# Optimization experiments

Hardware: AMD Instinct MI355X
Metric: run time of the kernel (lower is better)

The kernel has to match this reference:

```python
import jax, jax.numpy as jnp
import numpy as np

L = 10
DIM = 4
TABLE = 1 << 16
BASE_RES = 16.0
PLS = 2.0
HID = 64
SCALE_MULTI = 0.5
DENSITY_OFFSET = -1.0
SCENE_SCALING = 2.0
PRIMES = (np.uint32(1), np.uint32(2654435761), np.uint32(805459861))


def _safe_exp(x):
    return jnp.exp(jnp.clip(x, -30.0, 10.0))


def _l2norm(x, eps=1e-8):
    return x / jnp.sqrt(jnp.sum(x * x, -1, keepdims=True) + eps)


def _circumcenters(tets):
    # tets: [T,4,3]; solve 2(vi-v0).c = |vi|^2-|v0|^2
    v0 = tets[:, 0]
    A = 2.0 * (tets[:, 1:] - v0[:, None, :]) + 1e-6 * jnp.eye(3, dtype=tets.dtype)
    b = jnp.sum(tets[:, 1:] ** 2, -1) - jnp.sum(v0 ** 2, -1)[:, None]
    c = jnp.linalg.solve(A, b[..., None])[..., 0]
    r = jnp.linalg.norm(c - v0, axis=-1)
    return c, r


def _project_to_tet(p, tets):
    # clamp-and-renormalize barycentric coordinates (approximate projection)
    v0 = tets[:, 0]
    E = tets[:, 1:] - v0[:, None, :]
    M = jnp.einsum('tid,tjd->tij', E, E) + 1e-6 * jnp.eye(3, dtype=tets.dtype)
    rhs = jnp.einsum('tid,td->ti', E, p - v0)
    lam = jnp.linalg.solve(M, rhs[..., None])[..., 0]
    bary = jnp.concatenate([1.0 - lam.sum(-1, keepdims=True), lam], -1)
    bary = jnp.clip(bary, 0.0, 1.0)
    bary = bary / jnp.clip(bary.sum(-1, keepdims=True), 1e-6, None)
    return jnp.einsum('tv,tvd->td', bary, tets)


def _contract_mean_std(x, std):
    # mipnerf-360 style scene contraction of mean; std scaled by |J| ~ 1/n^2
    n = jnp.maximum(jnp.linalg.norm(x, axis=-1, keepdims=True), 1e-9)
    cx = jnp.where(n <= 1.0, x, (2.0 - 1.0 / n) * x / n)
    cs = std * jnp.where(n[..., 0] <= 1.0, 1.0, 1.0 / (n[..., 0] ** 2))
    return cx, cs


def _hash_encode(pos, tables):
    # pos [T,3] in [0,1); tables [L, TABLE, DIM]; multiresolution hash grid
    mask = np.uint32(TABLE - 1)
    pos = jnp.clip(pos, 0.0, 1.0 - 1e-6)
    feats = []
    for l in range(L):
        res = float(np.floor(BASE_RES * (PLS ** l)))
        x = pos * res
        f = jnp.floor(x)
        w = x - f
        fi = f.astype(jnp.uint32)
        acc = jnp.zeros(pos.shape[:-1] + (DIM,), pos.dtype)
        for cz in (0, 1):
            for cy in (0, 1):
                for cx in (0, 1):
                    c = fi + jnp.asarray((cx, cy, cz), jnp.uint32)
                    h = ((c[..., 0] * PRIMES[0]) ^ (c[..., 1] * PRIMES[1]) ^ (c[..., 2] * PRIMES[2])) & mask
                    wt = ((w[..., 0] if cx else 1.0 - w[..., 0]) *
                          (w[..., 1] if cy else 1.0 - w[..., 1]) *
                          (w[..., 2] if cz else 1.0 - w[..., 2]))
                    acc = acc + tables[l][h.astype(jnp.int32)] * wt[..., None]
        feats.append(acc)
    return jnp.stack(feats, axis=1)  # [T, L, DIM]


def _forward(vertices, indices, center, tables, W1, b1, W2, b2, W3, b3):
    tets = vertices[indices]  # [T,4,3] gather
    cc, radius = _circumcenters(tets)
    cc = _project_to_tet(cc, tets)
    normalized = (cc - center) / SCENE_SCALING
    cv, cr = _contract_mean_std(normalized, radius / SCENE_SCALING)
    cr = cr * SCALE_MULTI
    n = jnp.arange(L, dtype=vertices.dtype)
    erf_x = 1.0 / jnp.sqrt(PLS * 4.0 * n[None, :] * cr[:, None] + 1e-12)
    scaling = jax.lax.erf(erf_x)  # [T, L] per-level erf anti-aliasing scale
    pos = cv * 0.25 + 0.5  # contracted [-2,2] -> [0,1]
    feats = _hash_encode(pos, tables) * scaling[..., None]
    h = feats.reshape(feats.shape[0], L * DIM)
    h = jax.nn.selu(h @ W1 + b1)
    h = jax.nn.selu(h @ W2 + b2)
    out = h @ W3 + b3  # [T, 13]
    density = _safe_exp(out[:, 0] + DENSITY_OFFSET)
    pairs = ((0, 1), (0, 2), (0, 3), (1, 2), (1, 3), (2, 3))
    el = jnp.stack([jnp.linalg.norm(tets[:, i] - tets[:, j], axis=1) for i, j in pairs], 0).max(0)
    alpha = 1.0 - jnp.exp(-density * el)
    V = vertices.shape[0]
    vertex_alpha = jnp.zeros((V,), vertices.dtype).at[indices].max(
        jnp.broadcast_to(alpha[:, None], indices.shape))  # scatter amax
    fs = out[:, 1:]
    base = fs[:, :3] + 0.5
    grads = jnp.clip(base[:, :, None], 0.0, None) * jnp.tanh(fs[:, 3:12].reshape(-1, 3, 3))
    offs = _l2norm(tets - cc[:, None, :])
    vcol = base[:, None, :] + jnp.einsum('tcd,tvd->tvc', grads, offs)  # [T,4,3]
    return vertex_alpha, vcol


def setup_inputs() -> dict:
    key = jax.random.key(0)
    ks = jax.random.split(key, 8)
    V, T = 100000, 500000
    vertices = jax.random.normal(ks[0], (V, 3), jnp.float32) * 0.5
    indices = jax.random.randint(ks[1], (T, 4), 0, V, jnp.int32)
    center = jnp.zeros((1, 3), jnp.float32)
    tables = jax.random.normal(ks[2], (L, TABLE, DIM), jnp.float32) * 1e-2
    def lin(k, i, o):
        s = (6.0 / (i + o)) ** 0.5
        return jax.random.uniform(k, (i, o), jnp.float32, -s, s)
    return dict(vertices=vertices, indices=indices, center=center, tables=tables,
                W1=lin(ks[3], L * DIM, HID), b1=jnp.zeros((HID,), jnp.float32),
                W2=lin(ks[4], HID, HID), b2=jnp.zeros((HID,), jnp.float32),
                W3=lin(ks[5], HID, 13), b3=jnp.zeros((13,), jnp.float32))


def reference(vertices, indices, center, tables, W1, b1, W2, b2, W3, b3):
    return _forward(vertices, indices, center, tables, W1, b1, W2, b2, W3, b3)
```

## Files before the change

kernel.cpp:

```cpp
#include <hip/hip_runtime.h>
#include <math.h>

#define NLVL 10
#define TBL 65536
#define NHID 64
#define NIN 40
#define LDP 68

typedef __attribute__((ext_vector_type(8))) short bf16x8;
typedef __attribute__((ext_vector_type(4))) float f32x4;
typedef unsigned int uint;
typedef unsigned short ushort;

__device__ __forceinline__ float selu_f(float x) {
    return 1.0507009873554805f * (x > 0.0f ? x : 1.6732632423543772f * (__expf(x) - 1.0f));
}
__device__ __forceinline__ float fast_tanh(float x) {
    float xx = fminf(fmaxf(x, -15.0f), 15.0f);
    float t = __expf(2.0f * xx);
    return (t - 1.0f) / (t + 1.0f);
}
__device__ __forceinline__ short2 tsplit(float x) {
    uint u = __float_as_uint(x);
    short hi = (short)(u >> 16);
    float hif = __uint_as_float(u & 0xFFFF0000u);
    float lo = x - hif;
    short los = (short)(__float_as_uint(lo) >> 16);
    short2 s; s.x = hi; s.y = los;
    return s;
}

__device__ __forceinline__ void solve3d(const double A[3][3], const double b[3], double x[3]) {
    double a00=A[0][0], a01=A[0][1], a02=A[0][2];
    double a10=A[1][0], a11=A[1][1], a12=A[1][2];
    double a20=A[2][0], a21=A[2][1], a22=A[2][2];
    double C00 =  (a11*a22 - a12*a21);
    double C01 = -(a10*a22 - a12*a20);
    double C02 =  (a10*a21 - a11*a20);
    double C10 = -(a01*a22 - a02*a21);
    double C11 =  (a00*a22 - a02*a20);
    double C12 = -(a00*a21 - a01*a20);
    double C20 =  (a01*a12 - a02*a11);
    double C21 = -(a00*a12 - a02*a10);
    double C22 =  (a00*a11 - a01*a10);
    double det = a00*C00 + a01*C01 + a02*C02;
    double inv = 1.0 / det;
    x[0] = (C00*b[0] + C10*b[1] + C20*b[2]) * inv;
    x[1] = (C01*b[0] + C11*b[1] + C21*b[2]) * inv;
    x[2] = (C02*b[0] + C12*b[1] + C22*b[2]) * inv;
}

__global__ void __launch_bounds__(256) zero_alpha_kernel(float* out, int V) {
    int i = blockIdx.x * blockDim.x + threadIdx.x;
    if (i < V) out[i] = 0.0f;
}

__device__ __forceinline__ void enc2(const float4* __restrict__ tb4,
                                     float px, float py, float pz, float crf,
                                     int l0, float f[8]) {
    uint idx[2][8];
    float wt[2][8];
    #pragma unroll
    for (int h = 0; h < 2; ++h) {
        int l = l0 + h;
        float res = (float)(16 << l);
        float x0 = px*res, x1 = py*res, x2 = pz*res;
        float f0 = floorf(x0), f1 = floorf(x1), f2 = floorf(x2);
        float w0 = x0-f0, w1 = x1-f1, w2 = x2-f2;
        uint i0 = (uint)f0, i1 = (uint)f1, i2 = (uint)f2;
        #pragma unroll
        for (int cn = 0; cn < 8; ++cn) {
            uint cx = (uint)(cn & 1), cy = (uint)((cn >> 1) & 1), cz = (uint)((cn >> 2) & 1);
            idx[h][cn] = (((i0 + cx) * 1u) ^ ((i1 + cy) * 2654435761u) ^ ((i2 + cz) * 805459861u)) & 65535u;
            wt[h][cn] = (cx ? w0 : 1.0f - w0) * (cy ? w1 : 1.0f - w1) * (cz ? w2 : 1.0f - w2);
        }
    }
    float4 v[2][8];
    #pragma unroll
    for (int h = 0; h < 2; ++h)
        #pragma unroll
        for (int cn = 0; cn < 8; ++cn)
            v[h][cn] = tb4[(size_t)(l0+h)*TBL + idx[h][cn]];
    #pragma unroll
    for (int h = 0; h < 2; ++h) {
        float a0=0.f, a1=0.f, a2=0.f, a3=0.f;
        #pragma unroll
        for (int cn = 0; cn < 8; ++cn) {
            float w = wt[h][cn];
            a0 = fmaf(v[h][cn].x, w, a0);
            a1 = fmaf(v[h][cn].y, w, a1);
            a2 = fmaf(v[h][cn].z, w, a2);
            a3 = fmaf(v[h][cn].w, w, a3);
        }
        float sc = erff(rsqrtf(8.0f*(float)(l0+h)*crf + 1e-12f));
        f[h*4+0] = a0*sc; f[h*4+1] = a1*sc; f[h*4+2] = a2*sc; f[h*4+3] = a3*sc;
    }
}

__device__ __forceinline__ void store_split8(const float f[8],
                                             ushort* __restrict__ fh,
                                             ushort* __restrict__ fl) {
    bf16x8 h8, l8;
    #pragma unroll
    for (int j = 0; j < 8; ++j) {
        short2 sp = tsplit(f[j]);
        h8[j] = sp.x; l8[j] = sp.y;
    }
    *reinterpret_cast<bf16x8*>(fh) = h8;
    *reinterpret_cast<bf16x8*>(fl) = l8;
}

__global__ void __launch_bounds__(256) geom01_kernel(
    const float* __restrict__ vertices,
    const int*   __restrict__ indices,
    const float* __restrict__ center,
    const float* __restrict__ tables,
    float* __restrict__ aux,
    ushort* __restrict__ feats_hi,
    ushort* __restrict__ feats_lo, int T)
{
    int t = blockIdx.x * blockDim.x + threadIdx.x;
    if (t >= T) return;

    double p[4][3];
    #pragma unroll
    for (int v = 0; v < 4; ++v) {
        int vid = indices[t*4+v];
        p[v][0] = (double)vertices[vid*3+0];
        p[v][1] = (double)vertices[vid*3+1];
        p[v][2] = (double)vertices[vid*3+2];
    }

    double A[3][3], bb[3];
    double v0sq = p[0][0]*p[0][0] + p[0][1]*p[0][1] + p[0][2]*p[0][2];
    #pragma unroll
    for (int i = 0; i < 3; ++i) {
        #pragma unroll
        for (int j = 0; j < 3; ++j)
            A[i][j] = 2.0*(p[i+1][j] - p[0][j]) + (i==j ? 1e-6 : 0.0);
        bb[i] = p[i+1][0]*p[i+1][0] + p[i+1][1]*p[i+1][1] + p[i+1][2]*p[i+1][2] - v0sq;
    }
    double c[3];
    solve3d(A, bb, c);
    double dx0 = c[0]-p[0][0], dy0 = c[1]-p[0][1], dz0 = c[2]-p[0][2];
    double radius = sqrt(dx0*dx0 + dy0*dy0 + dz0*dz0);

    double E[3][3];
    #pragma unroll
    for (int i = 0; i < 3; ++i)
        #pragma unroll
        for (int j = 0; j < 3; ++j)
            E[i][j] = p[i+1][j] - p[0][j];
    double M[3][3], rhs[3];
    #pragma unroll
    for (int i = 0; i < 3; ++i) {
        #pragma unroll
        for (int k = 0; k < 3; ++k)
            M[i][k] = E[i][0]*E[k][0] + E[i][1]*E[k][1] + E[i][2]*E[k][2] + (i==k ? 1e-6 : 0.0);
        rhs[i] = E[i][0]*dx0 + E[i][1]*dy0 + E[i][2]*dz0;
    }
    double lam[3];
    solve3d(M, rhs, lam);
    double bary[4];
    bary[0] = 1.0 - lam[0] - lam[1] - lam[2];
    bary[1] = lam[0]; bary[2] = lam[1]; bary[3] = lam[2];
    double bs = 0.0;
    #pragma unroll
    for (int v = 0; v < 4; ++v) {
        bary[v] = fmin(fmax(bary[v], 0.0), 1.0);
        bs += bary[v];
    }
    bs = fmax(bs, 1e-6);
    double cc[3];
    #pragma unroll
    for (int j = 0; j < 3; ++j)
        cc[j] = (bary[0]*p[0][j] + bary[1]*p[1][j] + bary[2]*p[2][j] + bary[3]*p[3][j]) / bs;

    double xv[3];
    xv[0] = (cc[0] - (double)center[0]) * 0.5;
    xv[1] = (cc[1] - (double)center[1]) * 0.5;
    xv[2] = (cc[2] - (double)center[2]) * 0.5;
    double nrm = sqrt(xv[0]*xv[0] + xv[1]*xv[1] + xv[2]*xv[2]);
    double n = fmax(nrm, 1e-9);
    double cv[3], cs;
    if (n <= 1.0) {
        cv[0]=xv[0]; cv[1]=xv[1]; cv[2]=xv[2];
        cs = radius * 0.5;
    } else {
        double f = (2.0 - 1.0/n) / n;
        cv[0]=xv[0]*f; cv[1]=xv[1]*f; cv[2]=xv[2]*f;
        cs = radius * 0.5 / (n*n);
    }
    float crf = (float)(cs * 0.5);

    float px = fminf(fmaxf((float)(cv[0]*0.25 + 0.5), 0.0f), 1.0f - 1e-6f);
    float py = fminf(fmaxf((float)(cv[1]*0.25 + 0.5), 0.0f), 1.0f - 1e-6f);
    float pz = fminf(fmaxf((float)(cv[2]*0.25 + 0.5), 0.0f), 1.0f - 1e-6f);

    float el = 0.0f;
    #pragma unroll
    for (int a = 0; a < 3; ++a)
        #pragma unroll
        for (int bq = a+1; bq < 4; ++bq) {
            float ddx = (float)(p[a][0]-p[bq][0]);
            float ddy = (float)(p[a][1]-p[bq][1]);
            float ddz = (float)(p[a][2]-p[bq][2]);
            el = fmaxf(el, sqrtf(ddx*ddx + ddy*ddy + ddz*ddz));
        }

    size_t st = (size_t)T;
    aux[0*st + t] = px;
    aux[1*st + t] = py;
    aux[2*st + t] = pz;
    aux[3*st + t] = crf;
    aux[4*st + t] = (float)cc[0];
    aux[5*st + t] = (float)cc[1];
    aux[6*st + t] = (float)cc[2];
    aux[7*st + t] = el;

    const float4* tb4 = reinterpret_cast<const float4*>(tables);
    float f01[8];
    enc2(tb4, px, py, pz, crf, 0, f01);
    store_split8(f01, feats_hi + (size_t)t*NIN, feats_lo + (size_t)t*NIN);
}

template<int L0>
__global__ void __launch_bounds__(256) hash_pass_kernel(
    const float* __restrict__ tables,
    const float* __restrict__ aux,
    ushort* __restrict__ feats_hi,
    ushort* __restrict__ feats_lo, int T)
{
    int t = blockIdx.x * blockDim.x + threadIdx.x;
    if (t >= T) return;
    size_t st = (size_t)T;
    float px = aux[0*st + t];
    float py = aux[1*st + t];
    float pz = aux[2*st + t];
    float crf = aux[3*st + t];
    const float4* tb4 = reinterpret_cast<const float4*>(tables);

    float f[8];
    enc2(tb4, px, py, pz, crf, L0, f);
    store_split8(f, feats_hi + (size_t)t*NIN + L0*4, feats_lo + (size_t)t*NIN + L0*4);
}

__global__ void __launch_bounds__(256, 2) mlp_mfma_kernel(
    const ushort* __restrict__ feats_hi,
    const ushort* __restrict__ feats_lo,
    const float* __restrict__ aux,
    const float* __restrict__ vertices,
    const int*   __restrict__ indices,
    const float* __restrict__ W1, const float* __restrict__ b1,
    const float* __restrict__ W2, const float* __restrict__ b2,
    const float* __restrict__ W3, const float* __restrict__ b3,
    float* __restrict__ out, int T, int V)
{
    __shared__ __align__(16) float hts[4][16][LDP];

    const int tid  = threadIdx.x;
    const int wid  = tid >> 6;
    const int lane = tid & 63;
    const int r    = lane & 15;
    const int g    = lane >> 4;

    bf16x8 w1h[2][4];
    bf16x8 w1l0[4];
    #pragma unroll
    for (int s = 0; s < 2; ++s)
        #pragma unroll
        for (int nt = 0; nt < 4; ++nt) {
            bf16x8 h, lo;
            #pragma unroll
            for (int j = 0; j < 8; ++j) {
                int k = s*32 + g*8 + j;
                float w = (k < NIN) ? W1[k*NHID + nt*16 + r] : 0.0f;
                short2 sp = tsplit(w);
                h[j] = sp.x; lo[j] = sp.y;
            }
            w1h[s][nt] = h;
            if (s == 0) w1l0[nt] = lo;
        }
    bf16x8 w2h[2][4], w2l[2][4];
    #pragma unroll
    for (int s = 0; s < 2; ++s)
        #pragma unroll
        for (int nt = 0; nt < 4; ++nt) {
            bf16x8 h, lo;
            #pragma unroll
            for (int j = 0; j < 8; ++j) {
                int k = s*32 + g*8 + j;
                float w = W2[k*NHID + nt*16 + r];
                short2 sp = tsplit(w);
                h[j] = sp.x; lo[j] = sp.y;
            }
            w2h[s][nt] = h; w2l[s][nt] = lo;
        }
    bf16x8 w3h[2], w3l[2];
    #pragma unroll
    for (int s = 0; s < 2; ++s) {
        bf16x8 h, lo;
        #pragma unroll
        for (int j = 0; j < 8; ++j) {
            int k = s*32 + g*8 + j;
            float w = (r < 13) ? W3[k*13 + r] : 0.0f;
            short2 sp = tsplit(w);
            h[j] = sp.x; lo[j] = sp.y;
        }
        w3h[s] = h; w3l[s] = lo;
    }
    float b1v[4], b2v[4];
    #pragma unroll
    for (int nt = 0; nt < 4; ++nt) { b1v[nt] = b1[nt*16 + r]; b2v[nt] = b2[nt*16 + r]; }
    float b3v = (r < 13) ? b3[r] : 0.0f;

    const size_t st = (size_t)T;
    const int nmt = (T + 15) >> 4;
    const int gw = blockIdx.x * 4 + wid;
    const int gstride = gridDim.x * 4;

    for (int mt = gw; mt < nmt; mt += gstride) {
        const int t0 = mt * 16;
        const int trow = t0 + r;
        const bool rowok = trow < T;

        bf16x8 ah0, al0, ah1;
        {
            const bf16x8 z = {0,0,0,0,0,0,0,0};
            const ushort* fh = feats_hi + (size_t)trow * NIN;
            const ushort* fl = feats_lo + (size_t)trow * NIN;
            ah0 = rowok ? *reinterpret_cast<const bf16x8*>(fh + g*8) : z;
            al0 = rowok ? *reinterpret_cast<const bf16x8*>(fl + g*8) : z;
            ah1 = (rowok && g == 0) ? *reinterpret_cast<const bf16x8*>(fh + 32) : z;
        }

        #pragma unroll
        for (int nt = 0; nt < 4; ++nt) {
            f32x4 acc = {0.f, 0.f, 0.f, 0.f};
            acc = __builtin_amdgcn_mfma_f32_16x16x32_bf16(ah0, w1h[0][nt], acc, 0, 0, 0);
            acc = __builtin_amdgcn_mfma_f32_16x16x32_bf16(ah0, w1l0[nt],  acc, 0, 0, 0);
            acc = __builtin_amdgcn_mfma_f32_16x16x32_bf16(al0, w1h[0][nt], acc, 0, 0, 0);
            acc = __builtin_amdgcn_mfma_f32_16x16x32_bf16(ah1, w1h[1][nt], acc, 0, 0, 0);
            #pragma unroll
            for (int q = 0; q < 4; ++q)
                hts[wid][g*4 + q][nt*16 + r] = selu_f(acc[q] + b1v[nt]);
        }
        asm volatile("s_waitcnt lgkmcnt(0)" ::: "memory");

        bf16x8 a2h[2], a2l[2];
        #pragma unroll
        for (int s = 0; s < 2; ++s) {
            float4 u0 = *reinterpret_cast<const float4*>(&hts[wid][r][s*32 + g*8]);
            float4 u1 = *reinterpret_cast<const float4*>(&hts[wid][r][s*32 + g*8 + 4]);
            bf16x8 h, lo;
            short2 sp;
            sp = tsplit(u0.x); h[0]=sp.x; lo[0]=sp.y;
            sp = tsplit(u0.y); h[1]=sp.x; lo[1]=sp.y;
            sp = tsplit(u0.z); h[2]=sp.x; lo[2]=sp.y;
            sp = tsplit(u0.w); h[3]=sp.x; lo[3]=sp.y;
            sp = tsplit(u1.x); h[4]=sp.x; lo[4]=sp.y;
            sp = tsplit(u1.y); h[5]=sp.x; lo[5]=sp.y;
            sp = tsplit(u1.z); h[6]=sp.x; lo[6]=sp.y;
            sp = tsplit(u1.w); h[7]=sp.x; lo[7]=sp.y;
            a2h[s] = h; a2l[s] = lo;
        }
        asm volatile("s_waitcnt lgkmcnt(0)" ::: "memory");
        float h2v[4][4];
        #pragma unroll
        for (int nt = 0; nt < 4; ++nt) {
            f32x4 acc = {0.f, 0.f, 0.f, 0.f};
            #pragma unroll
            for (int s = 0; s < 2; ++s) {
                acc = __builtin_amdgcn_mfma_f32_16x16x32_bf16(a2h[s], w2h[s][nt], acc, 0, 0, 0);
                acc = __builtin_amdgcn_mfma_f32_16x16x32_bf16(a2h[s], w2l[s][nt], acc, 0, 0, 0);
                acc = __builtin_amdgcn_mfma_f32_16x16x32_bf16(a2l[s], w2h[s][nt], acc, 0, 0, 0);
            }
            #pragma unroll
            for (int q = 0; q < 4; ++q) h2v[nt][q] = selu_f(acc[q] + b2v[nt]);
        }
        #pragma unroll
        for (int nt = 0; nt < 4; ++nt)
            #pragma unroll
            for (int q = 0; q < 4; ++q)
                hts[wid][g*4 + q][nt*16 + r] = h2v[nt][q];
        asm volatile("s_waitcnt lgkmcnt(0)" ::: "memory");

        bf16x8 a3h[2], a3l[2];
        #pragma unroll
        for (int s = 0; s < 2; ++s) {
            float4 u0 = *reinterpret_cast<const float4*>(&hts[wid][r][s*32 + g*8]);
            float4 u1 = *reinterpret_cast<const float4*>(&hts[wid][r][s*32 + g*8 + 4]);
            bf16x8 h, lo;
            short2 sp;
            sp = tsplit(u0.x); h[0]=sp.x; lo[0]=sp.y;
            sp = tsplit(u0.y); h[1]=sp.x; lo[1]=sp.y;
            sp = tsplit(u0.z); h[2]=sp.x; lo[2]=sp.y;
            sp = tsplit(u0.w); h[3]=sp.x; lo[3]=sp.y;
            sp = tsplit(u1.x); h[4]=sp.x; lo[4]=sp.y;
            sp = tsplit(u1.y); h[5]=sp.x; lo[5]=sp.y;
            sp = tsplit(u1.z); h[6]=sp.x; lo[6]=sp.y;
            sp = tsplit(u1.w); h[7]=sp.x; lo[7]=sp.y;
            a3h[s] = h; a3l[s] = lo;
        }
        asm volatile("s_waitcnt lgkmcnt(0)" ::: "memory");
        {
            f32x4 acc = {0.f, 0.f, 0.f, 0.f};
            #pragma unroll
            for (int s = 0; s < 2; ++s) {
                acc = __builtin_amdgcn_mfma_f32_16x16x32_bf16(a3h[s], w3h[s], acc, 0, 0, 0);
                acc = __builtin_amdgcn_mfma_f32_16x16x32_bf16(a3h[s], w3l[s], acc, 0, 0, 0);
                acc = __builtin_amdgcn_mfma_f32_16x16x32_bf16(a3l[s], w3h[s], acc, 0, 0, 0);
            }
            #pragma unroll
            for (int q = 0; q < 4; ++q)
                hts[wid][g*4 + q][r] = acc[q] + b3v;
        }
        asm volatile("s_waitcnt lgkmcnt(0)" ::: "memory");

        {
            int et = lane >> 2;
            int ev = lane & 3;
            int te = t0 + et;
            if (te < T) {
                const float* orow = hts[wid][et];
                float4 o0 = *reinterpret_cast<const float4*>(&orow[0]);
                float4 o1 = *reinterpret_cast<const float4*>(&orow[4]);
                float4 o2 = *reinterpret_cast<const float4*>(&orow[8]);
                float o12 = orow[12];

                float el  = aux[7*st + te];
                float cc0 = aux[4*st + te], cc1 = aux[5*st + te], cc2 = aux[6*st + te];

                float dv = fminf(fmaxf(o0.x - 1.0f, -30.0f), 10.0f);
                float density = __expf(dv);
                float alpha = 1.0f - __expf(-density * el);
                int ab = __float_as_int(alpha);
                int vid = indices[te*4 + ev];
                atomicMax((int*)out + vid, ab);

                float base0 = o0.y + 0.5f, base1 = o0.z + 0.5f, base2 = o0.w + 0.5f;
                float bc0 = fmaxf(base0, 0.0f), bc1 = fmaxf(base1, 0.0f), bc2 = fmaxf(base2, 0.0f);
                float g00 = bc0*fast_tanh(o1.x), g01 = bc0*fast_tanh(o1.y), g02 = bc0*fast_tanh(o1.z);
                float g10 = bc1*fast_tanh(o1.w), g11 = bc1*fast_tanh(o2.x), g12 = bc1*fast_tanh(o2.y);
                float g20 = bc2*fast_tanh(o2.z), g21 = bc2*fast_tanh(o2.w), g22 = bc2*fast_tanh(o12);

                float pxv = vertices[vid*3+0], pyv = vertices[vid*3+1], pzv = vertices[vid*3+2];
                float ox = pxv-cc0, oy = pyv-cc1, oz = pzv-cc2;
                float inv = rsqrtf(ox*ox + oy*oy + oz*oz + 1e-8f);
                float q0 = ox*inv, q1 = oy*inv, q2 = oz*inv;
                float* vout = out + V + (size_t)te * 12 + ev*3;
                vout[0] = base0 + g00*q0 + g01*q1 + g02*q2;
                vout[1] = base1 + g10*q0 + g11*q1 + g12*q2;
                vout[2] = base2 + g20*q0 + g21*q1 + g22*q2;
            }
        }
        asm volatile("s_waitcnt lgkmcnt(0)" ::: "memory");
    }
}

__global__ void __launch_bounds__(256) tet_forward_fused(
    const float* __restrict__ vertices,
    const int*   __restrict__ indices,
    const float* __restrict__ center,
    const float* __restrict__ tables,
    const float* __restrict__ W1, const float* __restrict__ b1,
    const float* __restrict__ W2, const float* __restrict__ b2,
    const float* __restrict__ W3, const float* __restrict__ b3,
    float* __restrict__ out, int T, int V)
{
    int t = blockIdx.x * blockDim.x + threadIdx.x;
    if (t >= T) return;

    double p[4][3];
    int vv[4];
    #pragma unroll
    for (int v = 0; v < 4; ++v) {
        vv[v] = indices[t*4+v];
        p[v][0] = (double)vertices[vv[v]*3+0];
        p[v][1] = (double)vertices[vv[v]*3+1];
        p[v][2] = (double)vertices[vv[v]*3+2];
    }
    double A[3][3], bb[3];
    double v0sq = p[0][0]*p[0][0] + p[0][1]*p[0][1] + p[0][2]*p[0][2];
    #pragma unroll
    for (int i = 0; i < 3; ++i) {
        #pragma unroll
        for (int j = 0; j < 3; ++j)
            A[i][j] = 2.0*(p[i+1][j] - p[0][j]) + (i==j ? 1e-6 : 0.0);
        bb[i] = p[i+1][0]*p[i+1][0] + p[i+1][1]*p[i+1][1] + p[i+1][2]*p[i+1][2] - v0sq;
    }
    double c[3];
    solve3d(A, bb, c);
    double dx0 = c[0]-p[0][0], dy0 = c[1]-p[0][1], dz0 = c[2]-p[0][2];
    double radius = sqrt(dx0*dx0 + dy0*dy0 + dz0*dz0);
    double E[3][3];
    #pragma unroll
    for (int i = 0; i < 3; ++i)
        #pragma unroll
        for (int j = 0; j < 3; ++j)
            E[i][j] = p[i+1][j] - p[0][j];
    double M[3][3], rhs[3];
    #pragma unroll
    for (int i = 0; i < 3; ++i) {
        #pragma unroll
        for (int k = 0; k < 3; ++k)
            M[i][k] = E[i][0]*E[k][0] + E[i][1]*E[k][1] + E[i][2]*E[k][2] + (i==k ? 1e-6 : 0.0);
        rhs[i] = E[i][0]*dx0 + E[i][1]*dy0 + E[i][2]*dz0;
    }
    double lam[3];
    solve3d(M, rhs, lam);
    double bary[4];
    bary[0] = 1.0 - lam[0] - lam[1] - lam[2];
    bary[1] = lam[0]; bary[2] = lam[1]; bary[3] = lam[2];
    double bs = 0.0;
    #pragma unroll
    for (int v = 0; v < 4; ++v) { bary[v] = fmin(fmax(bary[v], 0.0), 1.0); bs += bary[v]; }
    bs = fmax(bs, 1e-6);
    double cc[3];
    #pragma unroll
    for (int j = 0; j < 3; ++j)
        cc[j] = (bary[0]*p[0][j] + bary[1]*p[1][j] + bary[2]*p[2][j] + bary[3]*p[3][j]) / bs;
    double xv[3];
    xv[0] = (cc[0] - (double)center[0]) * 0.5;
    xv[1] = (cc[1] - (double)center[1]) * 0.5;
    xv[2] = (cc[2] - (double)center[2]) * 0.5;
    double nrm = sqrt(xv[0]*xv[0] + xv[1]*xv[1] + xv[2]*xv[2]);
    double n = fmax(nrm, 1e-9);
    double cv[3], cs;
    if (n <= 1.0) { cv[0]=xv[0]; cv[1]=xv[1]; cv[2]=xv[2]; cs = radius * 0.5; }
    else { double f = (2.0 - 1.0/n) / n; cv[0]=xv[0]*f; cv[1]=xv[1]*f; cv[2]=xv[2]*f; cs = radius * 0.5 / (n*n); }
    float crf = (float)(cs * 0.5);
    float pos0 = fminf(fmaxf((float)(cv[0]*0.25 + 0.5), 0.0f), 1.0f - 1e-6f);
    float pos1 = fminf(fmaxf((float)(cv[1]*0.25 + 0.5), 0.0f), 1.0f - 1e-6f);
    float pos2 = fminf(fmaxf((float)(cv[2]*0.25 + 0.5), 0.0f), 1.0f - 1e-6f);

    float h0[NIN];
    float res = 16.0f;
    #pragma unroll
    for (int l = 0; l < NLVL; ++l) {
        float x0 = pos0*res, x1 = pos1*res, x2 = pos2*res;
        float f0 = floorf(x0), f1 = floorf(x1), f2 = floorf(x2);
        float w0 = x0-f0, w1 = x1-f1, w2 = x2-f2;
        unsigned i0 = (unsigned)f0, i1 = (unsigned)f1, i2 = (unsigned)f2;
        float a0=0.f, a1=0.f, a2=0.f, a3=0.f;
        #pragma unroll
        for (int cn = 0; cn < 8; ++cn) {
            unsigned cx = (unsigned)(cn & 1), cy = (unsigned)((cn >> 1) & 1), cz = (unsigned)((cn >> 2) & 1);
            unsigned hh = ((i0 + cx) * 1u) ^ ((i1 + cy) * 2654435761u) ^ ((i2 + cz) * 805459861u);
            hh &= 65535u;
            float wt = (cx ? w0 : 1.0f - w0) * (cy ? w1 : 1.0f - w1) * (cz ? w2 : 1.0f - w2);
            const float4 tv = *reinterpret_cast<const float4*>(tables + ((size_t)l*TBL + hh)*4);
            a0 = fmaf(tv.x, wt, a0); a1 = fmaf(tv.y, wt, a1);
            a2 = fmaf(tv.z, wt, a2); a3 = fmaf(tv.w, wt, a3);
        }
        float sc = erff(rsqrtf(8.0f*(float)l*crf + 1e-12f));
        h0[l*4+0] = a0*sc; h0[l*4+1] = a1*sc; h0[l*4+2] = a2*sc; h0[l*4+3] = a3*sc;
        res *= 2.0f;
    }

    float h1[NHID];
    #pragma unroll
    for (int j = 0; j < NHID; ++j) h1[j] = b1[j];
    #pragma unroll
    for (int i = 0; i < NIN; ++i) {
        float hi = h0[i];
        #pragma unroll
        for (int j = 0; j < NHID; ++j) h1[j] = fmaf(hi, W1[i*NHID + j], h1[j]);
    }
    #pragma unroll
    for (int j = 0; j < NHID; ++j) h1[j] = selu_f(h1[j]);

    float o[13];
    #pragma unroll
    for (int k = 0; k < 13; ++k) o[k] = b3[k];
    #pragma unroll
    for (int half = 0; half < 2; ++half) {
        float h2h[32];
        #pragma unroll
        for (int jj = 0; jj < 32; ++jj) h2h[jj] = b2[half*32 + jj];
        #pragma unroll
        for (int i = 0; i < NHID; ++i) {
            float hi = h1[i];
            #pragma unroll
            for (int jj = 0; jj < 32; ++jj)
                h2h[jj] = fmaf(hi, W2[i*NHID + half*32 + jj], h2h[jj]);
        }
        #pragma unroll
        for (int jj = 0; jj < 32; ++jj) {
            float hv = selu_f(h2h[jj]);
            #pragma unroll
            for (int k = 0; k < 13; ++k)
                o[k] = fmaf(hv, W3[(half*32 + jj)*13 + k], o[k]);
        }
    }

    float dv = fminf(fmaxf(o[0] - 1.0f, -30.0f), 10.0f);
    float density = __expf(dv);
    float el = 0.0f;
    #pragma unroll
    for (int a = 0; a < 3; ++a)
        #pragma unroll
        for (int bq = a+1; bq < 4; ++bq) {
            float ddx = (float)(p[a][0]-p[bq][0]);
            float ddy = (float)(p[a][1]-p[bq][1]);
            float ddz = (float)(p[a][2]-p[bq][2]);
            el = fmaxf(el, sqrtf(ddx*ddx + ddy*ddy + ddz*ddz));
        }
    float alpha = 1.0f - __expf(-density * el);
    int ab = __float_as_int(alpha);
    atomicMax((int*)out + vv[0], ab);
    atomicMax((int*)out + vv[1], ab);
    atomicMax((int*)out + vv[2], ab);
    atomicMax((int*)out + vv[3], ab);

    float base0 = o[1] + 0.5f, base1 = o[2] + 0.5f, base2 = o[3] + 0.5f;
    float bc0 = fmaxf(base0, 0.0f), bc1 = fmaxf(base1, 0.0f), bc2 = fmaxf(base2, 0.0f);
    float g00 = bc0*fast_tanh(o[4]),  g01 = bc0*fast_tanh(o[5]),  g02 = bc0*fast_tanh(o[6]);
    float g10 = bc1*fast_tanh(o[7]),  g11 = bc1*fast_tanh(o[8]),  g12 = bc1*fast_tanh(o[9]);
    float g20 = bc2*fast_tanh(o[10]), g21 = bc2*fast_tanh(o[11]), g22 = bc2*fast_tanh(o[12]);

    float* vout = out + V + (size_t)t * 12;
    #pragma unroll
    for (int v = 0; v < 4; ++v) {
        float ox = (float)(p[v][0]-cc[0]), oy = (float)(p[v][1]-cc[1]), oz = (float)(p[v][2]-cc[2]);
        float inv = rsqrtf(ox*ox + oy*oy + oz*oz + 1e-8f);
        float q0 = ox*inv, q1 = oy*inv, q2 = oz*inv;
        vout[v*3+0] = base0 + g00*q0 + g01*q1 + g02*q2;
        vout[v*3+1] = base1 + g10*q0 + g11*q1 + g12*q2;
        vout[v*3+2] = base2 + g20*q0 + g21*q1 + g22*q2;
    }
}

extern "C" void kernel_launch(void* const* d_in, const int* in_sizes, int n_in,
                              void* d_out, int out_size, void* d_ws, size_t ws_size,
                              hipStream_t stream) {
    const float* vertices = (const float*)d_in[0];
    const int*   indices  = (const int*)d_in[1];
    const float* center   = (const float*)d_in[2];
    const float* tables   = (const float*)d_in[3];
    const float* W1 = (const float*)d_in[4];
    const float* b1 = (const float*)d_in[5];
    const float* W2 = (const float*)d_in[6];
    const float* b2 = (const float*)d_in[7];
    const float* W3 = (const float*)d_in[8];
    const float* b3 = (const float*)d_in[9];
    int V = in_sizes[0] / 3;
    int T = in_sizes[1] / 4;
    float* out = (float*)d_out;

    hipLaunchKernelGGL(zero_alpha_kernel, dim3((V + 255) / 256), dim3(256), 0, stream, out, V);

    size_t need = (size_t)T * 48 * sizeof(float);
    dim3 grid((T + 255) / 256), blk(256);
    if (ws_size >= need) {
        float* aux = (float*)d_ws;
        ushort* feats_hi = (ushort*)(aux + (size_t)T * 8);
        ushort* feats_lo = feats_hi + (size_t)T * NIN;
        hipLaunchKernelGGL(geom01_kernel, grid, blk, 0, stream,
                           vertices, indices, center, tables, aux, feats_hi, feats_lo, T);
        hipLaunchKernelGGL((hash_pass_kernel<2>), grid, blk, 0, stream, tables, aux, feats_hi, feats_lo, T);
        hipLaunchKernelGGL((hash_pass_kernel<4>), grid, blk, 0, stream, tables, aux, feats_hi, feats_lo, T);
        hipLaunchKernelGGL((hash_pass_kernel<6>), grid, blk, 0, stream, tables, aux, feats_hi, feats_lo, T);
        hipLaunchKernelGGL((hash_pass_kernel<8>), grid, blk, 0, stream, tables, aux, feats_hi, feats_lo, T);
        hipLaunchKernelGGL(mlp_mfma_kernel, dim3(1024), blk, 0, stream, feats_hi, feats_lo, aux,
                           vertices, indices, W1, b1, W2, b2, W3, b3, out, T, V);
    } else {
        hipLaunchKernelGGL(tet_forward_fused, grid, blk, 0, stream,
                           vertices, indices, center, tables, W1, b1, W2, b2, W3, b3, out, T, V);
    }
}
```

Measured before the change: 236.8 us.

## Prefetch next tile features and epilogue gathers during MLP MFMA work

Software-pipelines the persistent MLP loop. Input feature fragments for the next tile are loaded while the current tile is being computed, and the per-tet indices, aux values and vertex gathers are issued early so their latency overlaps the MFMA layers. MFMA sections are also wrapped in s_setprio raises so their waves get issue priority. In exchange, more registers are live across the loop, which may lower occupancy.

```diff
diff --git a/kernel.cpp b/kernel.cpp
--- a/kernel.cpp
+++ b/kernel.cpp
@@ -318,22 +318,34 @@
     const int nmt = (T + 15) >> 4;
     const int gw = blockIdx.x * 4 + wid;
     const int gstride = gridDim.x * 4;
+    const bf16x8 zfrag = {0,0,0,0,0,0,0,0};
+
+    if (gw >= nmt) return;
+
+    bf16x8 ah0, al0, ah1;
+    {
+        int trow = gw*16 + r;
+        bool rowok = trow < T;
+        const ushort* fh = feats_hi + (size_t)trow * NIN;
+        const ushort* fl = feats_lo + (size_t)trow * NIN;
+        ah0 = rowok ? *reinterpret_cast<const bf16x8*>(fh + g*8) : zfrag;
+        al0 = rowok ? *reinterpret_cast<const bf16x8*>(fl + g*8) : zfrag;
+        ah1 = (rowok && g == 0) ? *reinterpret_cast<const bf16x8*>(fh + 32) : zfrag;
+    }
 
     for (int mt = gw; mt < nmt; mt += gstride) {
         const int t0 = mt * 16;
-        const int trow = t0 + r;
-        const bool rowok = trow < T;
-
-        bf16x8 ah0, al0, ah1;
-        {
-            const bf16x8 z = {0,0,0,0,0,0,0,0};
-            const ushort* fh = feats_hi + (size_t)trow * NIN;
-            const ushort* fl = feats_lo + (size_t)trow * NIN;
-            ah0 = rowok ? *reinterpret_cast<const bf16x8*>(fh + g*8) : z;
-            al0 = rowok ? *reinterpret_cast<const bf16x8*>(fl + g*8) : z;
-            ah1 = (rowok && g == 0) ? *reinterpret_cast<const bf16x8*>(fh + 32) : z;
-        }
-
+
+        const int te = t0 + (lane >> 2);
+        const int ev = lane & 3;
+        const bool teok = te < T;
+        int vid = teok ? indices[te*4 + ev] : 0;
+        float el  = teok ? aux[7*st + te] : 0.0f;
+        float cc0 = teok ? aux[4*st + te] : 0.0f;
+        float cc1 = teok ? aux[5*st + te] : 0.0f;
+        float cc2 = teok ? aux[6*st + te] : 0.0f;
+
+        __builtin_amdgcn_s_setprio(1);
         #pragma unroll
         for (int nt = 0; nt < 4; ++nt) {
             f32x4 acc = {0.f, 0.f, 0.f, 0.f};
@@ -345,6 +357,26 @@
             for (int q = 0; q < 4; ++q)
                 hts[wid][g*4 + q][nt*16 + r] = selu_f(acc[q] + b1v[nt]);
         }
+        __builtin_amdgcn_s_setprio(0);
+
+        const int mtn = mt + gstride;
+        bf16x8 nah0 = zfrag, nal0 = zfrag, nah1 = zfrag;
+        if (mtn < nmt) {
+            int trow = mtn*16 + r;
+            bool rowok = trow < T;
+            const ushort* fh = feats_hi + (size_t)trow * NIN;
+            const ushort* fl = feats_lo + (size_t)trow * NIN;
+            if (rowok) {
+                nah0 = *reinterpret_cast<const bf16x8*>(fh + g*8);
+                nal0 = *reinterpret_cast<const bf16x8*>(fl + g*8);
+                if (g == 0) nah1 = *reinterpret_cast<const bf16x8*>(fh + 32);
+            }
+        }
+
+        float pvx = vertices[vid*3+0];
+        float pvy = vertices[vid*3+1];
+        float pvz = vertices[vid*3+2];
+
         asm volatile("s_waitcnt lgkmcnt(0)" ::: "memory");
 
         bf16x8 a2h[2], a2l[2];
@@ -366,6 +398,7 @@
         }
         asm volatile("s_waitcnt lgkmcnt(0)" ::: "memory");
         float h2v[4][4];
+        __builtin_amdgcn_s_setprio(1);
         #pragma unroll
         for (int nt = 0; nt < 4; ++nt) {
             f32x4 acc = {0.f, 0.f, 0.f, 0.f};
@@ -378,6 +411,7 @@
             #pragma unroll
             for (int q = 0; q < 4; ++q) h2v[nt][q] = selu_f(acc[q] + b2v[nt]);
         }
+        __builtin_amdgcn_s_setprio(0);
         #pragma unroll
         for (int nt = 0; nt < 4; ++nt)
             #pragma unroll
@@ -405,56 +439,50 @@
         asm volatile("s_waitcnt lgkmcnt(0)" ::: "memory");
         {
             f32x4 acc = {0.f, 0.f, 0.f, 0.f};
+            __builtin_amdgcn_s_setprio(1);
             #pragma unroll
             for (int s = 0; s < 2; ++s) {
                 acc = __builtin_amdgcn_mfma_f32_16x16x32_bf16(a3h[s], w3h[s], acc, 0, 0, 0);
                 acc = __builtin_amdgcn_mfma_f32_16x16x32_bf16(a3h[s], w3l[s], acc, 0, 0, 0);
                 acc = __builtin_amdgcn_mfma_f32_16x16x32_bf16(a3l[s], w3h[s], acc, 0, 0, 0);
             }
+            __builtin_amdgcn_s_setprio(0);
             #pragma unroll
             for (int q = 0; q < 4; ++q)
                 hts[wid][g*4 + q][r] = acc[q] + b3v;
         }
         asm volatile("s_waitcnt lgkmcnt(0)" ::: "memory");
 
-        {
-            int et = lane >> 2;
-            int ev = lane & 3;
-            int te = t0 + et;
-            if (te < T) {
-                const float* orow = hts[wid][et];
-                float4 o0 = *reinterpret_cast<const float4*>(&orow[0]);
-                float4 o1 = *reinterpret_cast<const float4*>(&orow[4]);
-                float4 o2 = *reinterpret_cast<const float4*>(&orow[8]);
-                float o12 = orow[12];
-
-                float el  = aux[7*st + te];
-                float cc0 = aux[4*st + te], cc1 = aux[5*st + te], cc2 = aux[6*st + te];
-
-                float dv = fminf(fmaxf(o0.x - 1.0f, -30.0f), 10.0f);
-                float density = __expf(dv);
-                float alpha = 1.0f - __expf(-density * el);
-                int ab = __float_as_int(alpha);
-                int vid = indices[te*4 + ev];
-                atomicMax((int*)out + vid, ab);
-
-                float base0 = o0.y + 0.5f, base1 = o0.z + 0.5f, base2 = o0.w + 0.5f;
-                float bc0 = fmaxf(base0, 0.0f), bc1 = fmaxf(base1, 0.0f), bc2 = fmaxf(base2, 0.0f);
-                float g00 = bc0*fast_tanh(o1.x), g01 = bc0*fast_tanh(o1.y), g02 = bc0*fast_tanh(o1.z);
-                float g10 = bc1*fast_tanh(o1.w), g11 = bc1*fast_tanh(o2.x), g12 = bc1*fast_tanh(o2.y);
-                float g20 = bc2*fast_tanh(o2.z), g21 = bc2*fast_tanh(o2.w), g22 = bc2*fast_tanh(o12);
-
-                float pxv = vertices[vid*3+0], pyv = vertices[vid*3+1], pzv = vertices[vid*3+2];
-                float ox = pxv-cc0, oy = pyv-cc1, oz = pzv-cc2;
-                float inv = rsqrtf(ox*ox + oy*oy + oz*oz + 1e-8f);
-                float q0 = ox*inv, q1 = oy*inv, q2 = oz*inv;
-                float* vout = out + V + (size_t)te * 12 + ev*3;
-                vout[0] = base0 + g00*q0 + g01*q1 + g02*q2;
-                vout[1] = base1 + g10*q0 + g11*q1 + g12*q2;
-                vout[2] = base2 + g20*q0 + g21*q1 + g22*q2;
-            }
+        if (teok) {
+            const float* orow = hts[wid][lane >> 2];
+            float4 o0 = *reinterpret_cast<const float4*>(&orow[0]);
+            float4 o1 = *reinterpret_cast<const float4*>(&orow[4]);
+            float4 o2 = *reinterpret_cast<const float4*>(&orow[8]);
+            float o12 = orow[12];
+
+            float dv = fminf(fmaxf(o0.x - 1.0f, -30.0f), 10.0f);
+            float density = __expf(dv);
+            float alpha = 1.0f - __expf(-density * el);
+            int ab = __float_as_int(alpha);
+            atomicMax((int*)out + vid, ab);
+
+            float base0 = o0.y + 0.5f, base1 = o0.z + 0.5f, base2 = o0.w + 0.5f;
+            float bc0 = fmaxf(base0, 0.0f), bc1 = fmaxf(base1, 0.0f), bc2 = fmaxf(base2, 0.0f);
+            float g00 = bc0*fast_tanh(o1.x), g01 = bc0*fast_tanh(o1.y), g02 = bc0*fast_tanh(o1.z);
+            float g10 = bc1*fast_tanh(o1.w), g11 = bc1*fast_tanh(o2.x), g12 = bc1*fast_tanh(o2.y);
+            float g20 = bc2*fast_tanh(o2.z), g21 = bc2*fast_tanh(o2.w), g22 = bc2*fast_tanh(o12);
+
+            float ox = pvx-cc0, oy = pvy-cc1, oz = pvz-cc2;
+            float inv = rsqrtf(ox*ox + oy*oy + oz*oz + 1e-8f);
+            float q0 = ox*inv, q1 = oy*inv, q2 = oz*inv;
+            float* vout = out + V + (size_t)te * 12 + ev*3;
+            vout[0] = base0 + g00*q0 + g01*q1 + g02*q2;
+            vout[1] = base1 + g10*q0 + g11*q1 + g12*q2;
+            vout[2] = base2 + g20*q0 + g21*q1 + g22*q2;
         }
         asm volatile("s_waitcnt lgkmcnt(0)" ::: "memory");
+
+        ah0 = nah0; al0 = nal0; ah1 = nah1;
     }
 }
 
```

Measured after the change: 237.3 us. No clear change (+0.2%).
